# Kernel tuning notes

Measured on AMD Instinct MI355X. Metric: run time of the kernel, lower is better.

Reference implementation:

```python
import jax, jax.numpy as jnp
import numpy as np
from jax import lax

DN = ('NCH', 'OIH', 'NCH')

def _conv(x, w, b, pad):
    # x: [B, C, L]; replication (edge) pad then VALID conv, per nn.ReplicationPad1d + Conv1d
    if pad != (0, 0):
        x = jnp.pad(x, ((0, 0), (0, 0), pad), mode='edge')
    y = lax.conv_general_dilated(x, w, (1,), 'VALID', dimension_numbers=DN)
    return y + b[None, :, None]

def setup_inputs() -> dict:
    key = jax.random.key(0)
    ks = jax.random.split(key, 11)
    B, L, C, H = 32, 512, 300, 512
    s = 1.0 / np.sqrt(C)
    inp = {
        'x': jax.random.normal(ks[0], (B, L, C), jnp.float32),
        'w1': jax.random.normal(ks[1], (C, C, 1), jnp.float32) * s,
        'b1': jax.random.normal(ks[2], (C,), jnp.float32) * s,
        'w2': jax.random.normal(ks[3], (C, C, 2), jnp.float32) * s,
        'b2': jax.random.normal(ks[4], (C,), jnp.float32) * s,
        'w3': jax.random.normal(ks[5], (C, C, 3), jnp.float32) * s,
        'b3': jax.random.normal(ks[6], (C,), jnp.float32) * s,
        'w7': jax.random.normal(ks[7], (C, C, 7), jnp.float32) * s,
        'b7': jax.random.normal(ks[8], (C,), jnp.float32) * s,
        'slp_w': jax.random.normal(ks[9], (H, 5 * C), jnp.float32) * (1.0 / np.sqrt(5 * C)),
        'slp_b': jax.random.normal(ks[10], (H,), jnp.float32) * (1.0 / np.sqrt(5 * C)),
    }
    return inp

def reference(x, w1, b1, w2, b2, w3, b3, w7, b7, slp_w, slp_b):
    xc = jnp.transpose(x, (0, 2, 1))  # [B, C, L]
    x1 = jnp.tanh(_conv(xc, w1, b1, (0, 0)))
    x2 = jnp.tanh(_conv(xc, w2, b2, (0, 1)))
    x3 = jnp.tanh(_conv(xc, w3, b3, (1, 1)))
    x5 = x3  # faithful to the original bug: x5 = self.conv3(x)
    x7 = jnp.tanh(_conv(xc, w7, b7, (3, 3)))
    # concat channels -> [B, L, 1500], then linear + tanh -> [B, L, 512]
    h = jnp.concatenate([x1, x2, x3, x5, x7], axis=1)  # [B, 5C, L]
    h = jnp.transpose(h, (0, 2, 1))  # [B, L, 5C]
    out = jnp.tanh(jnp.einsum('blc,hc->blh', h, slp_w) + slp_b)
    return out
```

## Files before the change

kernel.cpp:

```cpp
#include <hip/hip_runtime.h>
#include <hip/hip_bf16.h>

typedef __attribute__((ext_vector_type(8))) short short8;
typedef __attribute__((ext_vector_type(16))) float floatx16;

#define Bn 32
#define Ln 512
#define Cn 300
#define Hn 512
#define Nn (Bn*Ln)
#define XBP 518
#define XBC 320
#define HK 1216
#define LDST 72

#define XSROWS 262
#define XSSZ (XSROWS*LDST)
#define HSROWS 128
#define HSSZ (HSROWS*LDST)

#define XB_OFF 0
#define XB_ELEMS (Bn*XBP*XBC)
#define WB_OFF (XB_OFF + XB_ELEMS)
#define WB_ELEMS 1597440
#define WC_OFF (WB_OFF + WB_ELEMS)
#define WC_ELEMS (Hn*HK)
#define HB_OFF (WC_OFF + WC_ELEMS)
#define HB_ELEMS (Nn*HK)

__device__ __forceinline__ float fast_tanh(float x) {
    float ax = __builtin_fabsf(x);
    float t  = __expf(-2.f * ax);
    float r  = __builtin_fmaf(-2.f * t, __frcp_rn(1.f + t), 1.f);
    return __builtin_copysignf(r, x);
}


__global__ void prep_x(const float* __restrict__ x, __hip_bfloat16* __restrict__ xb) {
    int idx = blockIdx.x * 256 + threadIdx.x;
    if (idx >= Bn * XBP * XBC) return;
    int c = idx % XBC;
    int t = idx / XBC;
    int p = t % XBP;
    int b = t / XBP;
    int l = p - 3;
    l = l < 0 ? 0 : (l > Ln - 1 ? Ln - 1 : l);
    float v = (c < Cn) ? x[(b * Ln + l) * Cn + c] : 0.f;
    xb[idx] = __float2bfloat16(v);
}

__global__ void prep_w(const float* __restrict__ w1, const float* __restrict__ w2,
                       const float* __restrict__ w3, const float* __restrict__ w7,
                       __hip_bfloat16* __restrict__ Wb) {
    int idx = blockIdx.x * 256 + threadIdx.x;
    if (idx >= WB_ELEMS) return;
    int r = idx, taps; const float* w;
    if (r < 122880)       { taps = 1; w = w1; }
    else if (r < 368640)  { taps = 2; w = w2; r -= 122880; }
    else if (r < 737280)  { taps = 3; w = w3; r -= 368640; }
    else                  { taps = 7; w = w7; r -= 737280; }
    int e    = r & 7;
    int lane = (r >> 3) & 63;
    int f    = (r >> 9) & 15;
    int rt   = r >> 13;
    int t    = rt % taps;
    int mc   = rt / taps;
    int ch   = mc % 5;
    int mt   = mc / 5;
    int ks = f >> 2, mq = f & 3;
    int m = mt * 128 + mq * 32 + (lane & 31);
    int c = ch * 64 + ks * 16 + (lane >> 5) * 8 + e;
    float v = (m < Cn && c < Cn) ? w[(m * Cn + c) * taps + t] : 0.f;
    Wb[idx] = __float2bfloat16(v);
}

__global__ void prep_wc(const float* __restrict__ slp_w, __hip_bfloat16* __restrict__ Wc) {
    int idx = blockIdx.x * 256 + threadIdx.x;
    if (idx >= Hn * HK) return;
    int e    = idx & 7;
    int lane = (idx >> 3) & 63;
    int f    = (idx >> 9) & 15;
    int mc   = idx >> 13;
    int ch   = mc % 19;
    int mt4  = mc / 19;
    int ks = f >> 2, mq = f & 3;
    int h = mt4 * 128 + mq * 32 + (lane & 31);
    int k = ch * 64 + ks * 16 + (lane >> 5) * 8 + e;
    const float* row = slp_w + h * 1500;
    float v;
    if (k < 600)       v = row[k];
    else if (k < 900)  v = row[k] + row[k + 300];
    else if (k < 1200) v = row[k + 300];
    else               v = 0.f;
    Wc[idx] = __float2bfloat16(v);
}

#define MFMA __builtin_amdgcn_mfma_f32_32x32x16_bf16

__global__ __launch_bounds__(256, 2) void conv_kernel(
        const __hip_bfloat16* __restrict__ xbg, const __hip_bfloat16* __restrict__ Wbg,
        const float* __restrict__ bias1, const float* __restrict__ bias2,
        const float* __restrict__ bias3, const float* __restrict__ bias7,
        __hip_bfloat16* __restrict__ hbuf) {
    __shared__ __align__(16) short xs[2 * XSSZ];

    const int tid  = threadIdx.x;
    const int lane = tid & 63;
    const int wave = tid >> 6;
    const int wn = wave & 1, wm = wave >> 1;
    const int lr = lane & 31;
    const int lk = (lane >> 5) << 3;

    const int nt  = blockIdx.x;
    const int my  = blockIdx.y;
    const int cid = 3 - my / 3;
    const int mt  = my % 3;

    const int taps  = (cid == 0) ? 1 : (cid == 1) ? 2 : (cid == 2) ? 3 : 7;
    const int lead  = (cid == 2) ? 1 : (cid == 3) ? 3 : 0;
    const int fbase = (cid == 0) ? 0 : (cid == 1) ? 122880 : (cid == 2) ? 368640 : 737280;

    const int b  = nt >> 1;
    const int l0 = (nt & 1) << 8;
    const short* xbs = (const short*)xbg + (b * XBP + l0) * XBC;
    const short* wsp = (const short*)Wbg + fbase + mt * taps * 40960;

    const int srow = tid >> 3;
    const int scc  = (tid & 7) << 3;

    floatx16 acc[4][2];
#pragma unroll
    for (int i = 0; i < 4; i++)
#pragma unroll
        for (int j = 0; j < 2; j++)
#pragma unroll
            for (int r = 0; r < 16; r++) acc[i][j][r] = 0.f;

#pragma unroll
    for (int i = 0; i < 9; ++i) {
        int row = srow + 32 * i;
        if (i < 8 || row < XSROWS)
            *(short8*)&xs[row * LDST + scc] = *(const short8*)&xbs[row * XBC + scc];
    }
    __syncthreads();

    for (int c5 = 0; c5 < 5; ++c5) {
        const short* cur = xs + (c5 & 1) * XSSZ;
        short8 st[9];
        if (c5 < 4) {
            const int c0n = (c5 + 1) * 64;
#pragma unroll
            for (int i = 0; i < 9; ++i) {
                int row = srow + 32 * i;
                if (i < 8 || row < XSROWS)
                    st[i] = *(const short8*)&xbs[row * XBC + c0n + scc];
            }
        }
        for (int t = 0; t < taps; ++t) {
            const short* wt = wsp + (c5 * taps + t) * 8192;
            const int ab = (wn * 128 + lr + (t - lead + 3)) * LDST + lk;
#pragma unroll
            for (int ks = 0; ks < 4; ++ks) {
                short8 bf0 = *(const short8*)&wt[(ks * 4 + wm * 2 + 0) * 512 + lane * 8];
                short8 bf1 = *(const short8*)&wt[(ks * 4 + wm * 2 + 1) * 512 + lane * 8];
                const int ko = ks * 16;
                short8 a0 = *(const short8*)&cur[ab + ko];
                short8 a1 = *(const short8*)&cur[ab + 32 * LDST + ko];
                short8 a2 = *(const short8*)&cur[ab + 64 * LDST + ko];
                short8 a3 = *(const short8*)&cur[ab + 96 * LDST + ko];
                acc[0][0] = MFMA(a0, bf0, acc[0][0], 0, 0, 0);
                acc[0][1] = MFMA(a0, bf1, acc[0][1], 0, 0, 0);
                acc[1][0] = MFMA(a1, bf0, acc[1][0], 0, 0, 0);
                acc[1][1] = MFMA(a1, bf1, acc[1][1], 0, 0, 0);
                acc[2][0] = MFMA(a2, bf0, acc[2][0], 0, 0, 0);
                acc[2][1] = MFMA(a2, bf1, acc[2][1], 0, 0, 0);
                acc[3][0] = MFMA(a3, bf0, acc[3][0], 0, 0, 0);
                acc[3][1] = MFMA(a3, bf1, acc[3][1], 0, 0, 0);
            }
        }
        if (c5 < 4) {
            short* nxt = xs + ((c5 + 1) & 1) * XSSZ;
#pragma unroll
            for (int i = 0; i < 9; ++i) {
                int row = srow + 32 * i;
                if (i < 8 || row < XSROWS)
                    *(short8*)&nxt[row * LDST + scc] = st[i];
            }
        }
        __syncthreads();
    }

    const float* bias = (cid == 0) ? bias1 : (cid == 1) ? bias2 : (cid == 2) ? bias3 : bias7;
#pragma unroll
    for (int mi = 0; mi < 2; ++mi) {
        int mloc = mt * 128 + wm * 64 + mi * 32 + lr;
        if (mloc < Cn) {
            float bv = bias[mloc];
            int col = cid * Cn + mloc;
#pragma unroll
            for (int ni = 0; ni < 4; ++ni) {
                floatx16 v = acc[ni][mi];
#pragma unroll
                for (int reg = 0; reg < 16; ++reg) {
                    int nl = wn * 128 + ni * 32 + (reg & 3) + ((reg >> 2) << 3) + ((lane >> 5) << 2);
                    int n = nt * 256 + nl;
                    hbuf[n * HK + col] = __float2bfloat16(fast_tanh(v[reg] + bv));
                }
            }
        }
    }
}

__global__ __launch_bounds__(256, 3) void linear_kernel(
        const __hip_bfloat16* __restrict__ hbufg, const __hip_bfloat16* __restrict__ Wcg,
        const float* __restrict__ slp_b, float* __restrict__ out) {
    __shared__ __align__(16) short hs[2 * HSSZ];

    const int tid  = threadIdx.x;
    const int lane = tid & 63;
    const int wave = tid >> 6;
    const int wn = wave & 1, wm = wave >> 1;
    const int lr = lane & 31;
    const int lk = (lane >> 5) << 3;

    const int nt  = blockIdx.x;
    const int mt4 = blockIdx.y;

    const short* hbp = (const short*)hbufg + nt * 128 * HK;
    const short* wcp = (const short*)Wcg + mt4 * 155648;

    const int srow = tid >> 3;
    const int scc  = (tid & 7) << 3;

    floatx16 acc[2][2];
#pragma unroll
    for (int i = 0; i < 2; i++)
#pragma unroll
        for (int j = 0; j < 2; j++)
#pragma unroll
            for (int r = 0; r < 16; r++) acc[i][j][r] = 0.f;

#pragma unroll
    for (int i = 0; i < 4; ++i) {
        int row = srow + 32 * i;
        *(short8*)&hs[row * LDST + scc] = *(const short8*)&hbp[row * HK + scc];
    }
    __syncthreads();

    for (int ch = 0; ch < 19; ++ch) {
        const short* cur = hs + (ch & 1) * HSSZ;
        short8 st[4];
        if (ch < 18) {
            const int c0n = (ch + 1) * 64;
#pragma unroll
            for (int i = 0; i < 4; ++i) {
                int row = srow + 32 * i;
                st[i] = *(const short8*)&hbp[row * HK + c0n + scc];
            }
        }
        const short* wt = wcp + ch * 8192;
        const int ab = (wn * 64 + lr) * LDST + lk;
#pragma unroll
        for (int ks = 0; ks < 4; ++ks) {
            short8 bf0 = *(const short8*)&wt[(ks * 4 + wm * 2 + 0) * 512 + lane * 8];
            short8 bf1 = *(const short8*)&wt[(ks * 4 + wm * 2 + 1) * 512 + lane * 8];
            const int ko = ks * 16;
            short8 a0 = *(const short8*)&cur[ab + ko];
            short8 a1 = *(const short8*)&cur[ab + 32 * LDST + ko];
            acc[0][0] = MFMA(a0, bf0, acc[0][0], 0, 0, 0);
            acc[0][1] = MFMA(a0, bf1, acc[0][1], 0, 0, 0);
            acc[1][0] = MFMA(a1, bf0, acc[1][0], 0, 0, 0);
            acc[1][1] = MFMA(a1, bf1, acc[1][1], 0, 0, 0);
        }
        if (ch < 18) {
            short* nxt = hs + ((ch + 1) & 1) * HSSZ;
#pragma unroll
            for (int i = 0; i < 4; ++i) {
                int row = srow + 32 * i;
                *(short8*)&nxt[row * LDST + scc] = st[i];
            }
        }
        __syncthreads();
    }

#pragma unroll
    for (int mi = 0; mi < 2; ++mi) {
        int h = mt4 * 128 + wm * 64 + mi * 32 + lr;
        float bv = slp_b[h];
#pragma unroll
        for (int ni = 0; ni < 2; ++ni) {
            floatx16 v = acc[ni][mi];
#pragma unroll
            for (int reg = 0; reg < 16; ++reg) {
                int nl = wn * 64 + ni * 32 + (reg & 3) + ((reg >> 2) << 3) + ((lane >> 5) << 2);
                int n = nt * 128 + nl;
                out[n * Hn + h] = fast_tanh(v[reg] + bv);
            }
        }
    }
}


extern "C" void kernel_launch(void* const* d_in, const int* in_sizes, int n_in,
                              void* d_out, int out_size, void* d_ws, size_t ws_size,
                              hipStream_t stream) {
    const float* x     = (const float*)d_in[0];
    const float* w1    = (const float*)d_in[1];
    const float* b1    = (const float*)d_in[2];
    const float* w2    = (const float*)d_in[3];
    const float* b2    = (const float*)d_in[4];
    const float* w3    = (const float*)d_in[5];
    const float* b3    = (const float*)d_in[6];
    const float* w7    = (const float*)d_in[7];
    const float* b7    = (const float*)d_in[8];
    const float* slp_w = (const float*)d_in[9];
    const float* slp_b = (const float*)d_in[10];

    __hip_bfloat16* wsb = (__hip_bfloat16*)d_ws;

    prep_x<<<(XB_ELEMS + 255) / 256, 256, 0, stream>>>(x, wsb + XB_OFF);
    prep_w<<<(WB_ELEMS + 255) / 256, 256, 0, stream>>>(w1, w2, w3, w7, wsb + WB_OFF);
    prep_wc<<<(WC_ELEMS + 255) / 256, 256, 0, stream>>>(slp_w, wsb + WC_OFF);

    conv_kernel<<<dim3(64, 12), 256, 0, stream>>>(wsb + XB_OFF, wsb + WB_OFF,
                                                  b1, b2, b3, b7, wsb + HB_OFF);
    linear_kernel<<<dim3(128, 4), 256, 0, stream>>>(wsb + HB_OFF, wsb + WC_OFF,
                                                    slp_b, (float*)d_out);
}
```

Before: 201.8 us.

## Merge prep kernels, template conv by taps, halve conv tile, prefetch weights into registers

```diff
diff --git a/kernel.cpp b/kernel.cpp
--- a/kernel.cpp
+++ b/kernel.cpp
@@ -12,21 +12,20 @@
 #define XBP 518
 #define XBC 320
 #define HK 1216
-#define LDST 72
-
-#define XSROWS 262
-#define XSSZ (XSROWS*LDST)
+#define LDSTC 72
+
+#define XROWS 134
+#define XSZ (XROWS*LDSTC)
 #define HSROWS 128
-#define HSSZ (HSROWS*LDST)
-
+#define HSSZ (HSROWS*LDSTC)
+
+#define XB_ELEMS (Bn*XBP*XBC)
+#define WB_ELEMS 1597440
+#define WC_ELEMS (Hn*HK)
 #define XB_OFF 0
-#define XB_ELEMS (Bn*XBP*XBC)
 #define WB_OFF (XB_OFF + XB_ELEMS)
-#define WB_ELEMS 1597440
 #define WC_OFF (WB_OFF + WB_ELEMS)
-#define WC_ELEMS (Hn*HK)
 #define HB_OFF (WC_OFF + WC_ELEMS)
-#define HB_ELEMS (Nn*HK)
 
 __device__ __forceinline__ float fast_tanh(float x) {
     float ax = __builtin_fabsf(x);
@@ -35,162 +34,155 @@
     return __builtin_copysignf(r, x);
 }
 
-
-__global__ void prep_x(const float* __restrict__ x, __hip_bfloat16* __restrict__ xb) {
+__global__ void prep_all(const float* __restrict__ x,
+                         const float* __restrict__ w1, const float* __restrict__ w2,
+                         const float* __restrict__ w3, const float* __restrict__ w7,
+                         const float* __restrict__ slp_w,
+                         __hip_bfloat16* __restrict__ wsb) {
     int idx = blockIdx.x * 256 + threadIdx.x;
-    if (idx >= Bn * XBP * XBC) return;
-    int c = idx % XBC;
-    int t = idx / XBC;
-    int p = t % XBP;
-    int b = t / XBP;
-    int l = p - 3;
-    l = l < 0 ? 0 : (l > Ln - 1 ? Ln - 1 : l);
-    float v = (c < Cn) ? x[(b * Ln + l) * Cn + c] : 0.f;
-    xb[idx] = __float2bfloat16(v);
-}
-
-__global__ void prep_w(const float* __restrict__ w1, const float* __restrict__ w2,
-                       const float* __restrict__ w3, const float* __restrict__ w7,
-                       __hip_bfloat16* __restrict__ Wb) {
-    int idx = blockIdx.x * 256 + threadIdx.x;
-    if (idx >= WB_ELEMS) return;
-    int r = idx, taps; const float* w;
-    if (r < 122880)       { taps = 1; w = w1; }
-    else if (r < 368640)  { taps = 2; w = w2; r -= 122880; }
-    else if (r < 737280)  { taps = 3; w = w3; r -= 368640; }
-    else                  { taps = 7; w = w7; r -= 737280; }
-    int e    = r & 7;
-    int lane = (r >> 3) & 63;
-    int f    = (r >> 9) & 15;
-    int rt   = r >> 13;
-    int t    = rt % taps;
-    int mc   = rt / taps;
-    int ch   = mc % 5;
-    int mt   = mc / 5;
-    int ks = f >> 2, mq = f & 3;
-    int m = mt * 128 + mq * 32 + (lane & 31);
-    int c = ch * 64 + ks * 16 + (lane >> 5) * 8 + e;
-    float v = (m < Cn && c < Cn) ? w[(m * Cn + c) * taps + t] : 0.f;
-    Wb[idx] = __float2bfloat16(v);
-}
-
-__global__ void prep_wc(const float* __restrict__ slp_w, __hip_bfloat16* __restrict__ Wc) {
-    int idx = blockIdx.x * 256 + threadIdx.x;
-    if (idx >= Hn * HK) return;
-    int e    = idx & 7;
-    int lane = (idx >> 3) & 63;
-    int f    = (idx >> 9) & 15;
-    int mc   = idx >> 13;
-    int ch   = mc % 19;
-    int mt4  = mc / 19;
-    int ks = f >> 2, mq = f & 3;
-    int h = mt4 * 128 + mq * 32 + (lane & 31);
-    int k = ch * 64 + ks * 16 + (lane >> 5) * 8 + e;
-    const float* row = slp_w + h * 1500;
-    float v;
-    if (k < 600)       v = row[k];
-    else if (k < 900)  v = row[k] + row[k + 300];
-    else if (k < 1200) v = row[k + 300];
-    else               v = 0.f;
-    Wc[idx] = __float2bfloat16(v);
+    if (idx < XB_ELEMS) {
+        int c = idx % XBC;
+        int t = idx / XBC;
+        int p = t % XBP;
+        int b = t / XBP;
+        int l = p - 3;
+        l = l < 0 ? 0 : (l > Ln - 1 ? Ln - 1 : l);
+        float v = (c < Cn) ? x[(b * Ln + l) * Cn + c] : 0.f;
+        wsb[idx] = __float2bfloat16(v);
+    } else if (idx < WB_OFF + WB_ELEMS) {
+        int r = idx - WB_OFF, taps; const float* w;
+        if (r < 122880)       { taps = 1; w = w1; }
+        else if (r < 368640)  { taps = 2; w = w2; r -= 122880; }
+        else if (r < 737280)  { taps = 3; w = w3; r -= 368640; }
+        else                  { taps = 7; w = w7; r -= 737280; }
+        int e    = r & 7;
+        int lane = (r >> 3) & 63;
+        int f    = (r >> 9) & 15;
+        int rt   = r >> 13;
+        int t    = rt % taps;
+        int mc   = rt / taps;
+        int ch   = mc % 5;
+        int mt   = mc / 5;
+        int ks = f >> 2, mq = f & 3;
+        int m = mt * 128 + mq * 32 + (lane & 31);
+        int c = ch * 64 + ks * 16 + (lane >> 5) * 8 + e;
+        float v = (m < Cn && c < Cn) ? w[(m * Cn + c) * taps + t] : 0.f;
+        wsb[idx] = __float2bfloat16(v);
+    } else if (idx < WC_OFF + WC_ELEMS) {
+        int r = idx - WC_OFF;
+        int e    = r & 7;
+        int lane = (r >> 3) & 63;
+        int f    = (r >> 9) & 15;
+        int mc   = r >> 13;
+        int ch   = mc % 19;
+        int mt4  = mc / 19;
+        int ks = f >> 2, mq = f & 3;
+        int h = mt4 * 128 + mq * 32 + (lane & 31);
+        int k = ch * 64 + ks * 16 + (lane >> 5) * 8 + e;
+        const float* row = slp_w + h * 1500;
+        float v;
+        if (k < 600)       v = row[k];
+        else if (k < 900)  v = row[k] + row[k + 300];
+        else if (k < 1200) v = row[k + 300];
+        else               v = 0.f;
+        wsb[idx] = __float2bfloat16(v);
+    }
 }
 
 #define MFMA __builtin_amdgcn_mfma_f32_32x32x16_bf16
 
-__global__ __launch_bounds__(256, 2) void conv_kernel(
-        const __hip_bfloat16* __restrict__ xbg, const __hip_bfloat16* __restrict__ Wbg,
-        const float* __restrict__ bias1, const float* __restrict__ bias2,
-        const float* __restrict__ bias3, const float* __restrict__ bias7,
-        __hip_bfloat16* __restrict__ hbuf) {
-    __shared__ __align__(16) short xs[2 * XSSZ];
-
+template<int TAPS, int LEAD>
+__device__ __forceinline__ void conv_body(
+        const short* __restrict__ xbs, const short* __restrict__ wsp,
+        const float* __restrict__ bias, int cid, int mt, int nt,
+        __hip_bfloat16* __restrict__ hbuf, short* xs) {
     const int tid  = threadIdx.x;
     const int lane = tid & 63;
     const int wave = tid >> 6;
     const int wn = wave & 1, wm = wave >> 1;
     const int lr = lane & 31;
     const int lk = (lane >> 5) << 3;
-
-    const int nt  = blockIdx.x;
-    const int my  = blockIdx.y;
-    const int cid = 3 - my / 3;
-    const int mt  = my % 3;
-
-    const int taps  = (cid == 0) ? 1 : (cid == 1) ? 2 : (cid == 2) ? 3 : 7;
-    const int lead  = (cid == 2) ? 1 : (cid == 3) ? 3 : 0;
-    const int fbase = (cid == 0) ? 0 : (cid == 1) ? 122880 : (cid == 2) ? 368640 : 737280;
-
-    const int b  = nt >> 1;
-    const int l0 = (nt & 1) << 8;
-    const short* xbs = (const short*)xbg + (b * XBP + l0) * XBC;
-    const short* wsp = (const short*)Wbg + fbase + mt * taps * 40960;
-
-    const int srow = tid >> 3;
-    const int scc  = (tid & 7) << 3;
-
-    floatx16 acc[4][2];
-#pragma unroll
-    for (int i = 0; i < 4; i++)
+    const int TRIG = (TAPS >= 3) ? TAPS - 2 : 0;
+
+    floatx16 acc[2][2];
+#pragma unroll
+    for (int i = 0; i < 2; i++)
 #pragma unroll
         for (int j = 0; j < 2; j++)
 #pragma unroll
             for (int r = 0; r < 16; r++) acc[i][j][r] = 0.f;
 
-#pragma unroll
-    for (int i = 0; i < 9; ++i) {
-        int row = srow + 32 * i;
-        if (i < 8 || row < XSROWS)
-            *(short8*)&xs[row * LDST + scc] = *(const short8*)&xbs[row * XBC + scc];
+    short8 bA[8], bB[8], st[5];
+
+#pragma unroll
+    for (int i = 0; i < 5; ++i) {
+        int j = tid + 256 * i;
+        if (i < 4 || j < 1072)
+            st[i] = *(const short8*)&xbs[(j >> 3) * XBC + ((j & 7) << 3)];
+    }
+#pragma unroll
+    for (int ks = 0; ks < 4; ++ks)
+#pragma unroll
+        for (int mf = 0; mf < 2; ++mf)
+            bA[ks * 2 + mf] = *(const short8*)&wsp[(ks * 4 + wm * 2 + mf) * 512 + lane * 8];
+#pragma unroll
+    for (int i = 0; i < 5; ++i) {
+        int j = tid + 256 * i;
+        if (i < 4 || j < 1072)
+            *(short8*)&xs[(j >> 3) * LDSTC + ((j & 7) << 3)] = st[i];
     }
     __syncthreads();
 
     for (int c5 = 0; c5 < 5; ++c5) {
-        const short* cur = xs + (c5 & 1) * XSSZ;
-        short8 st[9];
+        const short* cur = xs + (c5 & 1) * XSZ;
+        short* nxt = xs + ((c5 + 1) & 1) * XSZ;
+        const int c0n = (c5 + 1) * 64;
+#pragma unroll
+        for (int t = 0; t < TAPS; ++t) {
+            if (!(c5 == 4 && t == TAPS - 1)) {
+                const short* wtn = (t + 1 < TAPS) ? wsp + (c5 * TAPS + t + 1) * 8192
+                                                  : wsp + ((c5 + 1) * TAPS) * 8192;
+#pragma unroll
+                for (int ks = 0; ks < 4; ++ks)
+#pragma unroll
+                    for (int mf = 0; mf < 2; ++mf)
+                        bB[ks * 2 + mf] = *(const short8*)&wtn[(ks * 4 + wm * 2 + mf) * 512 + lane * 8];
+            }
+            if (t == TRIG && c5 < 4) {
+#pragma unroll
+                for (int i = 0; i < 5; ++i) {
+                    int j = tid + 256 * i;
+                    if (i < 4 || j < 1072)
+                        st[i] = *(const short8*)&xbs[(j >> 3) * XBC + c0n + ((j & 7) << 3)];
+                }
+            }
+            const int sh = t - LEAD + 3;
+            const int ar = (wn * 64 + lr + sh) * LDSTC + lk;
+#pragma unroll
+            for (int ks = 0; ks < 4; ++ks) {
+                short8 a0 = *(const short8*)&cur[ar + ks * 16];
+                short8 a1 = *(const short8*)&cur[ar + 32 * LDSTC + ks * 16];
+                acc[0][0] = MFMA(a0, bA[ks * 2 + 0], acc[0][0], 0, 0, 0);
+                acc[0][1] = MFMA(a0, bA[ks * 2 + 1], acc[0][1], 0, 0, 0);
+                acc[1][0] = MFMA(a1, bA[ks * 2 + 0], acc[1][0], 0, 0, 0);
+                acc[1][1] = MFMA(a1, bA[ks * 2 + 1], acc[1][1], 0, 0, 0);
+            }
+            if (!(c5 == 4 && t == TAPS - 1)) {
+#pragma unroll
+                for (int f = 0; f < 8; ++f) bA[f] = bB[f];
+            }
+        }
         if (c5 < 4) {
-            const int c0n = (c5 + 1) * 64;
-#pragma unroll
-            for (int i = 0; i < 9; ++i) {
-                int row = srow + 32 * i;
-                if (i < 8 || row < XSROWS)
-                    st[i] = *(const short8*)&xbs[row * XBC + c0n + scc];
-            }
-        }
-        for (int t = 0; t < taps; ++t) {
-            const short* wt = wsp + (c5 * taps + t) * 8192;
-            const int ab = (wn * 128 + lr + (t - lead + 3)) * LDST + lk;
-#pragma unroll
-            for (int ks = 0; ks < 4; ++ks) {
-                short8 bf0 = *(const short8*)&wt[(ks * 4 + wm * 2 + 0) * 512 + lane * 8];
-                short8 bf1 = *(const short8*)&wt[(ks * 4 + wm * 2 + 1) * 512 + lane * 8];
-                const int ko = ks * 16;
-                short8 a0 = *(const short8*)&cur[ab + ko];
-                short8 a1 = *(const short8*)&cur[ab + 32 * LDST + ko];
-                short8 a2 = *(const short8*)&cur[ab + 64 * LDST + ko];
-                short8 a3 = *(const short8*)&cur[ab + 96 * LDST + ko];
-                acc[0][0] = MFMA(a0, bf0, acc[0][0], 0, 0, 0);
-                acc[0][1] = MFMA(a0, bf1, acc[0][1], 0, 0, 0);
-                acc[1][0] = MFMA(a1, bf0, acc[1][0], 0, 0, 0);
-                acc[1][1] = MFMA(a1, bf1, acc[1][1], 0, 0, 0);
-                acc[2][0] = MFMA(a2, bf0, acc[2][0], 0, 0, 0);
-                acc[2][1] = MFMA(a2, bf1, acc[2][1], 0, 0, 0);
-                acc[3][0] = MFMA(a3, bf0, acc[3][0], 0, 0, 0);
-                acc[3][1] = MFMA(a3, bf1, acc[3][1], 0, 0, 0);
-            }
-        }
-        if (c5 < 4) {
-            short* nxt = xs + ((c5 + 1) & 1) * XSSZ;
-#pragma unroll
-            for (int i = 0; i < 9; ++i) {
-                int row = srow + 32 * i;
-                if (i < 8 || row < XSROWS)
-                    *(short8*)&nxt[row * LDST + scc] = st[i];
+#pragma unroll
+            for (int i = 0; i < 5; ++i) {
+                int j = tid + 256 * i;
+                if (i < 4 || j < 1072)
+                    *(short8*)&nxt[(j >> 3) * LDSTC + ((j & 7) << 3)] = st[i];
             }
         }
         __syncthreads();
     }
 
-    const float* bias = (cid == 0) ? bias1 : (cid == 1) ? bias2 : (cid == 2) ? bias3 : bias7;
 #pragma unroll
     for (int mi = 0; mi < 2; ++mi) {
         int mloc = mt * 128 + wm * 64 + mi * 32 + lr;
@@ -198,12 +190,12 @@
             float bv = bias[mloc];
             int col = cid * Cn + mloc;
 #pragma unroll
-            for (int ni = 0; ni < 4; ++ni) {
+            for (int ni = 0; ni < 2; ++ni) {
                 floatx16 v = acc[ni][mi];
 #pragma unroll
                 for (int reg = 0; reg < 16; ++reg) {
-                    int nl = wn * 128 + ni * 32 + (reg & 3) + ((reg >> 2) << 3) + ((lane >> 5) << 2);
-                    int n = nt * 256 + nl;
+                    int nl = wn * 64 + ni * 32 + (reg & 3) + ((reg >> 2) << 3) + ((lane >> 5) << 2);
+                    int n = nt * 128 + nl;
                     hbuf[n * HK + col] = __float2bfloat16(fast_tanh(v[reg] + bv));
                 }
             }
@@ -211,7 +203,30 @@
     }
 }
 
-__global__ __launch_bounds__(256, 3) void linear_kernel(
+__global__ __launch_bounds__(256, 2) void conv_kernel(
+        const __hip_bfloat16* __restrict__ xbg, const __hip_bfloat16* __restrict__ Wbg,
+        const float* __restrict__ bias1, const float* __restrict__ bias2,
+        const float* __restrict__ bias3, const float* __restrict__ bias7,
+        __hip_bfloat16* __restrict__ hbuf) {
+    __shared__ __align__(16) short xs[2 * XSZ];
+
+    const int nt = blockIdx.x;
+    const int my = blockIdx.y;
+    const int g  = my / 3;
+    const int mt = my % 3;
+
+    const int b  = nt >> 2;
+    const int l0 = (nt & 3) << 7;
+    const short* xbs = (const short*)xbg + (b * XBP + l0) * XBC;
+    const short* wb  = (const short*)Wbg;
+
+    if (g == 0)      conv_body<7, 3>(xbs, wb + 737280 + mt * 7 * 40960, bias7, 3, mt, nt, hbuf, xs);
+    else if (g == 1) conv_body<3, 1>(xbs, wb + 368640 + mt * 3 * 40960, bias3, 2, mt, nt, hbuf, xs);
+    else if (g == 2) conv_body<2, 0>(xbs, wb + 122880 + mt * 2 * 40960, bias2, 1, mt, nt, hbuf, xs);
+    else             conv_body<1, 0>(xbs, wb +      0 + mt * 1 * 40960, bias1, 0, mt, nt, hbuf, xs);
+}
+
+__global__ __launch_bounds__(256, 2) void linear_kernel(
         const __hip_bfloat16* __restrict__ hbufg, const __hip_bfloat16* __restrict__ Wcg,
         const float* __restrict__ slp_b, float* __restrict__ out) {
     __shared__ __align__(16) short hs[2 * HSSZ];
@@ -229,9 +244,8 @@
     const short* hbp = (const short*)hbufg + nt * 128 * HK;
     const short* wcp = (const short*)Wcg + mt4 * 155648;
 
-    const int srow = tid >> 3;
-    const int scc  = (tid & 7) << 3;
-
+    const int srow = tid >> 1;
+    const int scc  = (tid & 1) << 5;
     floatx16 acc[2][2];
 #pragma unroll
     for (int i = 0; i < 2; i++)
@@ -240,44 +254,60 @@
 #pragma unroll
             for (int r = 0; r < 16; r++) acc[i][j][r] = 0.f;
 
+    short8 bA[8], bB[8], st[4];
+    (void)srow; (void)scc;
+
 #pragma unroll
     for (int i = 0; i < 4; ++i) {
-        int row = srow + 32 * i;
-        *(short8*)&hs[row * LDST + scc] = *(const short8*)&hbp[row * HK + scc];
+        int j = tid + 256 * i;
+        st[i] = *(const short8*)&hbp[(j >> 3) * HK + ((j & 7) << 3)];
+    }
+#pragma unroll
+    for (int ks = 0; ks < 4; ++ks)
+#pragma unroll
+        for (int mf = 0; mf < 2; ++mf)
+            bA[ks * 2 + mf] = *(const short8*)&wcp[(ks * 4 + wm * 2 + mf) * 512 + lane * 8];
+#pragma unroll
+    for (int i = 0; i < 4; ++i) {
+        int j = tid + 256 * i;
+        *(short8*)&hs[(j >> 3) * LDSTC + ((j & 7) << 3)] = st[i];
     }
     __syncthreads();
 
     for (int ch = 0; ch < 19; ++ch) {
         const short* cur = hs + (ch & 1) * HSSZ;
-        short8 st[4];
+        short* nxt = hs + ((ch + 1) & 1) * HSSZ;
         if (ch < 18) {
+            const short* wtn = wcp + (ch + 1) * 8192;
+#pragma unroll
+            for (int ks = 0; ks < 4; ++ks)
+#pragma unroll
+                for (int mf = 0; mf < 2; ++mf)
+                    bB[ks * 2 + mf] = *(const short8*)&wtn[(ks * 4 + wm * 2 + mf) * 512 + lane * 8];
             const int c0n = (ch + 1) * 64;
 #pragma unroll
             for (int i = 0; i < 4; ++i) {
-                int row = srow + 32 * i;
-                st[i] = *(const short8*)&hbp[row * HK + c0n + scc];
-            }
-        }
-        const short* wt = wcp + ch * 8192;
-        const int ab = (wn * 64 + lr) * LDST + lk;
+                int j = tid + 256 * i;
+                st[i] = *(const short8*)&hbp[(j >> 3) * HK + c0n + ((j & 7) << 3)];
+            }
+        }
+        const int ar = (wn * 64 + lr) * LDSTC + lk;
 #pragma unroll
         for (int ks = 0; ks < 4; ++ks) {
-            short8 bf0 = *(const short8*)&wt[(ks * 4 + wm * 2 + 0) * 512 + lane * 8];
-            short8 bf1 = *(const short8*)&wt[(ks * 4 + wm * 2 + 1) * 512 + lane * 8];
-            const int ko = ks * 16;
-            short8 a0 = *(const short8*)&cur[ab + ko];
-            short8 a1 = *(const short8*)&cur[ab + 32 * LDST + ko];
-            acc[0][0] = MFMA(a0, bf0, acc[0][0], 0, 0, 0);
-            acc[0][1] = MFMA(a0, bf1, acc[0][1], 0, 0, 0);
-            acc[1][0] = MFMA(a1, bf0, acc[1][0], 0, 0, 0);
-            acc[1][1] = MFMA(a1, bf1, acc[1][1], 0, 0, 0);
+            short8 a0 = *(const short8*)&cur[ar + ks * 16];
+            short8 a1 = *(const short8*)&cur[ar + 32 * LDSTC + ks * 16];
+            acc[0][0] = MFMA(a0, bA[ks * 2 + 0], acc[0][0], 0, 0, 0);
+            acc[0][1] = MFMA(a0, bA[ks * 2 + 1], acc[0][1], 0, 0, 0);
+            acc[1][0] = MFMA(a1, bA[ks * 2 + 0], acc[1][0], 0, 0, 0);
+            acc[1][1] = MFMA(a1, bA[ks * 2 + 1], acc[1][1], 0, 0, 0);
         }
         if (ch < 18) {
-            short* nxt = hs + ((ch + 1) & 1) * HSSZ;
+#pragma unroll
+            for (int f = 0; f < 8; ++f) bA[f] = bB[f];
 #pragma unroll
             for (int i = 0; i < 4; ++i) {
-                int row = srow + 32 * i;
-                *(short8*)&nxt[row * LDST + scc] = st[i];
+                int j = tid + 256 * i;
+                *(short8*)&nxt[(j >> 3) * LDSTC + ((j & 7) << 3)] = st[i];
             }
         }
         __syncthreads();
@@ -318,12 +348,11 @@
 
     __hip_bfloat16* wsb = (__hip_bfloat16*)d_ws;
 
-    prep_x<<<(XB_ELEMS + 255) / 256, 256, 0, stream>>>(x, wsb + XB_OFF);
-    prep_w<<<(WB_ELEMS + 255) / 256, 256, 0, stream>>>(w1, w2, w3, w7, wsb + WB_OFF);
-    prep_wc<<<(WC_ELEMS + 255) / 256, 256, 0, stream>>>(slp_w, wsb + WC_OFF);
-
-    conv_kernel<<<dim3(64, 12), 256, 0, stream>>>(wsb + XB_OFF, wsb + WB_OFF,
-                                                  b1, b2, b3, b7, wsb + HB_OFF);
+    const int prep_total = XB_ELEMS + WB_ELEMS + WC_ELEMS;
+    prep_all<<<(prep_total + 255) / 256, 256, 0, stream>>>(x, w1, w2, w3, w7, slp_w, wsb);
+
+    conv_kernel<<<dim3(128, 12), 256, 0, stream>>>(wsb + XB_OFF, wsb + WB_OFF,
+                                                   b1, b2, b3, b7, wsb + HB_OFF);
     linear_kernel<<<dim3(128, 4), 256, 0, stream>>>(wsb + HB_OFF, wsb + WC_OFF,
                                                     slp_b, (float*)d_out);
 }
```

After: 187.3 us. -7.2%, faster.
